# Optimization experiments

Hardware: AMD Instinct MI355X
Metric: run time of the kernel (lower is better)

The kernel has to match this reference:

```python
import jax, jax.numpy as jnp
import numpy as np
from jax import lax

VOCAB = 50257
EMBED = 512
HIDDEN = 1024
SEQ = 512


def setup_inputs() -> dict:
    key = jax.random.key(0)
    ks = jax.random.split(key, 12)
    seq = jax.random.randint(ks[0], (1, SEQ), 0, VOCAB, dtype=jnp.int64 if jax.config.jax_enable_x64 else jnp.int32)
    # h0/c0 emulate xavier_uniform_ init of a [1, hidden] tensor
    bound_hc = float(np.sqrt(6.0 / (1 + HIDDEN)))
    h0 = jax.random.uniform(ks[1], (1, HIDDEN), jnp.float32, -bound_hc, bound_hc)
    c0 = jax.random.uniform(ks[2], (1, HIDDEN), jnp.float32, -bound_hc, bound_hc)
    # parameters
    emb_weight = jax.random.normal(ks[3], (VOCAB, EMBED), jnp.float32)  # nn.Embedding default N(0,1)
    k_lstm = float(1.0 / np.sqrt(HIDDEN))
    w_ih = jax.random.uniform(ks[4], (4 * HIDDEN, 2 * EMBED), jnp.float32, -k_lstm, k_lstm)
    w_hh = jax.random.uniform(ks[5], (4 * HIDDEN, HIDDEN), jnp.float32, -k_lstm, k_lstm)
    b_ih = jax.random.uniform(ks[6], (4 * HIDDEN,), jnp.float32, -k_lstm, k_lstm)
    b_hh = jax.random.uniform(ks[7], (4 * HIDDEN,), jnp.float32, -k_lstm, k_lstm)
    k_lin = k_lstm
    w_lin = jax.random.uniform(ks[8], (VOCAB, HIDDEN), jnp.float32, -k_lin, k_lin)
    b_lin = jax.random.uniform(ks[9], (VOCAB,), jnp.float32, -k_lin, k_lin)
    return {"sequence": seq, "h0": h0, "c0": c0, "emb_weight": emb_weight,
            "w_ih": w_ih, "w_hh": w_hh, "b_ih": b_ih, "b_hh": b_hh,
            "w_lin": w_lin, "b_lin": b_lin}


def _lstm_cell(x, h, c, w_ih, w_hh, b_ih, b_hh):
    # PyTorch LSTMCell gate order: i, f, g, o
    gates = x @ w_ih.T + b_ih + h @ w_hh.T + b_hh  # [1, 4H]
    i, f, g, o = jnp.split(gates, 4, axis=1)
    i = jax.nn.sigmoid(i)
    f = jax.nn.sigmoid(f)
    g = jnp.tanh(g)
    o = jax.nn.sigmoid(o)
    c2 = f * c + i * g
    h2 = o * jnp.tanh(c2)
    return h2, c2


def reference(sequence, h0, c0, emb_weight, w_ih, w_hh, b_ih, b_hh, w_lin, b_lin):
    tokens = sequence[0]  # [S]; module structurally assumes batch=1
    prev0 = jnp.zeros((1, emb_weight.shape[1]), dtype=emb_weight.dtype)
    out0 = jnp.zeros((1, w_lin.shape[0]), dtype=emb_weight.dtype)

    def step(carry, tok):
        h, c, prev, _ = carry
        embed = emb_weight[tok][None, :]                       # [1, E]
        x = jnp.concatenate([prev, embed], axis=1)             # [1, 2E]
        h2, c2 = _lstm_cell(x, h, c, w_ih, w_hh, b_ih, b_hh)
        out = h2 @ w_lin.T + b_lin                             # [1, V]
        prev2 = emb_weight[jnp.argmax(out, axis=1)]            # greedy feedback, [1, E]
        return (h2, c2, prev2, out), None

    (h, c, prev, out), _ = lax.scan(step, (h0, c0, prev0, out0), tokens)
    return out  # logits of the last timestep, [1, VOCAB]
```

## Files before the change

kernel.cpp:

```cpp
#include <hip/hip_runtime.h>
#include <float.h>

#define VOCAB 50257
#define EMBED 512
#define HIDDEN 1024
#define SEQLEN 512
#define XDIM 1024
#define NSW 1571
#define NGW 1024
#define CANDB 128
#define CANDR 512

typedef unsigned long long u64;
typedef unsigned int u32;
typedef unsigned short u16;

__device__ __forceinline__ u32 fmono(float f) {
  u32 b = __float_as_uint(f);
  return b ^ ((b & 0x80000000u) ? 0xFFFFFFFFu : 0x80000000u);
}
__device__ __forceinline__ float funmono(u32 v) {
  u32 b = (v & 0x80000000u) ? (v ^ 0x80000000u) : ~v;
  return __uint_as_float(b);
}

__device__ __forceinline__ float wave_reduce_sum(float v) {
#pragma unroll
  for (int off = 32; off > 0; off >>= 1) v += __shfl_down(v, off);
  return v;
}
__device__ __forceinline__ float wave_reduce_max_f(float v) {
#pragma unroll
  for (int off = 32; off > 0; off >>= 1) v = fmaxf(v, __shfl_down(v, off));
  return v;
}
__device__ __forceinline__ u64 wave_reduce_max_u64(u64 v) {
#pragma unroll
  for (int off = 32; off > 0; off >>= 1) {
    u64 o = __shfl_down(v, off);
    if (o > v) v = o;
  }
  return v;
}

__device__ __forceinline__ float dotf4(float4 a, float4 b) {
  return a.x * b.x + a.y * b.y + a.z * b.z + a.w * b.w;
}

__device__ __forceinline__ int dot4i8(u32 a, u32 b, int c) {
#if __has_builtin(__builtin_amdgcn_sdot4)
  return __builtin_amdgcn_sdot4(a, b, c, false);
#else
  int r = c;
#pragma unroll
  for (int i = 0; i < 4; ++i) {
    const int ai = (int)(a << (24 - 8 * i)) >> 24;
    const int bi = (int)(b << (24 - 8 * i)) >> 24;
    r += ai * bi;
  }
  return r;
#endif
}

__device__ __forceinline__ int q8c(float x, float invs) {
  float q = rintf(x * invs);
  q = fminf(127.0f, fmaxf(-127.0f, q));
  return (int)q;
}


__global__ void init_state(const float* __restrict__ h0, const float* __restrict__ c0,
                           float* __restrict__ hbufs, float* __restrict__ cbufs) {
  int i = threadIdx.x;
  if (i < HIDDEN) {
    hbufs[i] = h0[i];
    cbufs[i] = c0[i];
  }
}

__global__ __launch_bounds__(256)
void convert_i8(const float* __restrict__ wlin, const float* __restrict__ blin,
                u32* __restrict__ qw, float4* __restrict__ rc4) {
  const int row = (blockIdx.x << 2) + (threadIdx.x >> 6);
  const int lane = threadIdx.x & 63;
  if (row >= VOCAB) return;
  const float4* wr = (const float4*)(wlin + (size_t)row * HIDDEN);
  float4 w[4];
#pragma unroll
  for (int i = 0; i < 4; ++i) w[i] = wr[4 * lane + i];
  float m = 0.f;
#pragma unroll
  for (int i = 0; i < 4; ++i)
    m = fmaxf(m, fmaxf(fmaxf(fabsf(w[i].x), fabsf(w[i].y)),
                       fmaxf(fabsf(w[i].z), fabsf(w[i].w))));
  m = wave_reduce_max_f(m);
  m = __shfl(m, 0);
  m = fmaxf(m, 1e-30f);
  const float s_r = m * (1.0f / 127.0f);
  const float invs = 127.0f / m;
  uint4 o;
  float aa = 0.f;
  float dd = 0.f;
  {
    u32 word[4];
#pragma unroll
    for (int i = 0; i < 4; ++i) {
      const int q0 = q8c(w[i].x, invs), q1 = q8c(w[i].y, invs);
      const int q2 = q8c(w[i].z, invs), q3 = q8c(w[i].w, invs);
      aa += (float)(abs(q0) + abs(q1) + abs(q2) + abs(q3));
      const float d0 = w[i].x - s_r * (float)q0, d1 = w[i].y - s_r * (float)q1;
      const float d2 = w[i].z - s_r * (float)q2, d3 = w[i].w - s_r * (float)q3;
      dd += d0 * d0 + d1 * d1 + d2 * d2 + d3 * d3;
      word[i] = (u32)(q0 & 0xFF) | ((u32)(q1 & 0xFF) << 8) |
                ((u32)(q2 & 0xFF) << 16) | ((u32)q3 << 24);
    }
    o.x = word[0]; o.y = word[1]; o.z = word[2]; o.w = word[3];
  }
  ((uint4*)(qw + (size_t)row * 256))[lane] = o;
  aa = wave_reduce_sum(aa);
  dd = wave_reduce_sum(dd);
  if (lane == 0)
    rc4[row] = make_float4(s_r, aa, sqrtf(dd) * 1.0000002f, blin[row]);
}

__global__ __launch_bounds__(256)
void gates_init(const float* __restrict__ wih, const float* __restrict__ whh,
                const float* __restrict__ bih, const float* __restrict__ bhh,
                const float* __restrict__ emb, const int* __restrict__ seq,
                const float* __restrict__ hbufs, float* __restrict__ gp) {
  __shared__ __align__(16) float xs2[EMBED];
  __shared__ __align__(16) float hs2[HIDDEN];
  const int tid = threadIdx.x;
  const int lane = tid & 63;
  const int wid = tid >> 6;
  const int tok = seq[0];
  for (int i = tid; i < EMBED; i += 256) xs2[i] = emb[(size_t)tok * EMBED + i];
  for (int i = tid; i < HIDDEN; i += 256) hs2[i] = hbufs[i];
  __syncthreads();

  const int row = (blockIdx.x << 2) + wid;
  const float4* wr = (const float4*)(wih + (size_t)row * XDIM);
  const float4* hr = (const float4*)(whh + (size_t)row * HIDDEN);
  float a = 0.f;
#pragma unroll
  for (int i = 0; i < 2; ++i) {
    const int k = lane + i * 64;
    a += dotf4(wr[128 + k], *((const float4*)&xs2[k * 4]));
  }
#pragma unroll
  for (int i = 0; i < 4; ++i) {
    const int k = lane + i * 64;
    a += dotf4(hr[k], *((const float4*)&hs2[k * 4]));
  }
  a = wave_reduce_sum(a);
  if (lane == 0) gp[row] = a + bih[row] + bhh[row];
}


__global__ __launch_bounds__(256)
void lstm_thin(const float* __restrict__ emb, const float* __restrict__ wih,
               const float* __restrict__ wlin, const float* __restrict__ blin,
               const float* __restrict__ gp,
               float* __restrict__ hbufs, float* __restrict__ cbufs,
               const u64* __restrict__ slotLo, const float* __restrict__ slotUp,
               const float* __restrict__ Lb, int t) {
  __shared__ __align__(16) float xs[EMBED];
  __shared__ __align__(16) float hs[HIDDEN];
  __shared__ u64 mred[4];
  __shared__ u64 bred[4];
  __shared__ int listb[CANDB];
  __shared__ int listr[CANDR];
  __shared__ int cntb, cntr;
  __shared__ int ptokS;

  const int tid = threadIdx.x;
  const int lane = tid & 63;
  const int wid = tid >> 6;

  const float* hin = hbufs + (t & 1) * HIDDEN;
  const float* cin = cbufs + (t & 1) * HIDDEN;
  float* hout = hbufs + ((t + 1) & 1) * HIDDEN;
  float* cout = cbufs + ((t + 1) & 1) * HIDDEN;

  const u64* sLo = slotLo + ((t + 1) & 1) * NSW;
  const float* sUp = slotUp + ((t + 1) & 1) * NSW;

  const int j = (blockIdx.x << 2) + wid;

  float4 wv[8];
  if (t > 0) {
#pragma unroll
    for (int g = 0; g < 4; ++g) {
      const float4* wr = (const float4*)(wih + (size_t)(g * HIDDEN + j) * XDIM);
      wv[2 * g] = wr[lane];
      wv[2 * g + 1] = wr[lane + 64];
    }
  }

  u64 v = 0;
  if (t > 0) {
#pragma unroll
    for (int k = 0; k < 7; ++k) {
      const int i = tid + (k << 8);
      if (i < NSW) {
        const u64 p = sLo[i];
        if (p > v) v = p;
      }
    }
  }

  ((float4*)hs)[tid] = ((const float4*)hin)[tid];

  int ptok = 0;
  if (t > 0) {
    v = wave_reduce_max_u64(v);
    if (lane == 0) mred[wid] = v;
    if (tid == 0) { cntb = 0; cntr = 0; }
    __syncthreads();
    u64 m = mred[0];
    if (mred[1] > m) m = mred[1];
    if (mred[2] > m) m = mred[2];
    if (mred[3] > m) m = mred[3];
    const float thrv = funmono((u32)(m >> 32));

#pragma unroll
    for (int k = 0; k < 7; ++k) {
      const int i = tid + (k << 8);
      if (i < NSW && sUp[i] >= thrv) {
        int ix = atomicAdd(&cntb, 1);
        if (ix < CANDB) listb[ix] = i;
      }
    }
    __syncthreads();
    const int nb = (cntb < CANDB) ? cntb : CANDB;

    for (int idx = tid; idx < nb * 32; idx += 256) {
      const int row = listb[idx >> 5] * 32 + (idx & 31);
      if (row < VOCAB && Lb[row] >= thrv) {
        int ix = atomicAdd(&cntr, 1);
        if (ix < CANDR) listr[ix] = row;
      }
    }
    __syncthreads();
    const int nr = (cntr < CANDR) ? cntr : CANDR;

    u64 best = 0;
    for (int ci = wid; ci < nr; ci += 4) {
      const int row = listr[ci];
      const float4* wr = (const float4*)(wlin + (size_t)row * HIDDEN);
      float a = 0.f;
#pragma unroll
      for (int i = 0; i < 4; ++i) {
        const int k = lane + i * 64;
        a += dotf4(wr[k], *((const float4*)&hs[k * 4]));
      }
      a = wave_reduce_sum(a);
      if (lane == 0) {
        const u64 pk = ((u64)fmono(a + blin[row]) << 32) | (u32)(VOCAB - row);
        if (pk > best) best = pk;
      }
    }
    if (lane == 0) bred[wid] = best;
    __syncthreads();
    if (tid == 0) {
      u64 b = bred[0];
      if (bred[1] > b) b = bred[1];
      if (bred[2] > b) b = bred[2];
      if (bred[3] > b) b = bred[3];
      ptokS = VOCAB - (int)(u32)(b & 0xFFFFFFFFu);
    }
    __syncthreads();
    ptok = ptokS;
  }

  if (t > 0) {
    for (int i = tid; i < EMBED; i += 256) xs[i] = emb[(size_t)ptok * EMBED + i];
  }
  __syncthreads();

  float ag[4] = {0.f, 0.f, 0.f, 0.f};
  if (t > 0) {
    const float4 xv0 = *((const float4*)&xs[lane * 4]);
    const float4 xv1 = *((const float4*)&xs[(lane + 64) * 4]);
#pragma unroll
    for (int g = 0; g < 4; ++g)
      ag[g] = dotf4(wv[2 * g], xv0) + dotf4(wv[2 * g + 1], xv1);
#pragma unroll
    for (int off = 32; off > 0; off >>= 1) {
#pragma unroll
      for (int g = 0; g < 4; ++g) ag[g] += __shfl_down(ag[g], off);
    }
  }

  if (lane == 0) {
    const float gi = gp[j] + ag[0];
    const float gf = gp[HIDDEN + j] + ag[1];
    const float gg = gp[2 * HIDDEN + j] + ag[2];
    const float go = gp[3 * HIDDEN + j] + ag[3];
    const float si = 1.0f / (1.0f + expf(-gi));
    const float sf = 1.0f / (1.0f + expf(-gf));
    const float tg = tanhf(gg);
    const float so = 1.0f / (1.0f + expf(-go));
    const float c2 = sf * cin[j] + si * tg;
    const float h2 = so * tanhf(c2);
    cout[j] = c2;
    hout[j] = h2;
  }
}

__global__ __launch_bounds__(256, 4)
void screen_gp(const u32* __restrict__ qw, const float4* __restrict__ rc4,
               const float* __restrict__ wih, const float* __restrict__ whh,
               const float* __restrict__ bih, const float* __restrict__ bhh,
               const float* __restrict__ emb, const int* __restrict__ seq,
               const float* __restrict__ hbufs, float* __restrict__ Lb,
               u64* __restrict__ slotLo, float* __restrict__ slotUp,
               float* __restrict__ gp, int t) {
  __shared__ __align__(16) float4 hs4[256];
  __shared__ __align__(16) u32 qhw[256];
  __shared__ __align__(16) u32 qh2w[256];
  __shared__ __align__(16) float xs2[EMBED];
  __shared__ float redm[4], reda[4], reds[4];
  __shared__ u64 redLo[4];
  __shared__ float redUp[4];

  const int tid = threadIdx.x;
  const int lane = tid & 63;
  const int wid = tid >> 6;
  const int bid = blockIdx.x;
  const int par = t & 1;

  const float* h = hbufs + ((t + 1) & 1) * HIDDEN;

  if (bid < NSW) {
    const float4 hv = ((const float4*)h)[tid];
    float m = fmaxf(fmaxf(fabsf(hv.x), fabsf(hv.y)), fmaxf(fabsf(hv.z), fabsf(hv.w)));
    float sa = fabsf(hv.x) + fabsf(hv.y) + fabsf(hv.z) + fabsf(hv.w);
    float ss = dotf4(hv, hv);
    m = wave_reduce_max_f(m);
    sa = wave_reduce_sum(sa);
    ss = wave_reduce_sum(ss);
    if (lane == 0) { redm[wid] = m; reda[wid] = sa; reds[wid] = ss; }
    __syncthreads();
    float maxh = fmaxf(fmaxf(redm[0], redm[1]), fmaxf(redm[2], redm[3]));
    maxh = fmaxf(maxh, 1e-30f);
    const float SumAbsH = reda[0] + reda[1] + reda[2] + reda[3];
    const float NormH = sqrtf(reds[0] + reds[1] + reds[2] + reds[3]) * 1.0000002f;
    const float s_h = maxh * (1.0f / 127.0f);
    const float s2 = s_h * (1.0f / 254.0f);
    const float inv_sh = 127.0f / maxh;
    const float inv_s2 = 254.0f * inv_sh;
    {
      const int qa = q8c(hv.x, inv_sh), qb = q8c(hv.y, inv_sh);
      const int qc = q8c(hv.z, inv_sh), qd = q8c(hv.w, inv_sh);
      const float ra = hv.x - s_h * (float)qa, rb = hv.y - s_h * (float)qb;
      const float rcr = hv.z - s_h * (float)qc, rd = hv.w - s_h * (float)qd;
      const int pa = q8c(ra, inv_s2), pb = q8c(rb, inv_s2);
      const int pc = q8c(rcr, inv_s2), pd = q8c(rd, inv_s2);
      qhw[tid] = (u32)(qa & 0xFF) | ((u32)(qb & 0xFF) << 8) |
                 ((u32)(qc & 0xFF) << 16) | ((u32)qd << 24);
      qh2w[tid] = (u32)(pa & 0xFF) | ((u32)(pb & 0xFF) << 8) |
                  ((u32)(pc & 0xFF) << 16) | ((u32)pd << 24);
    }
    __syncthreads();
    const uint4 qh = ((const uint4*)qhw)[lane];
    const uint4 qh2 = ((const uint4*)qh2w)[lane];

    const int row0 = bid * 32 + wid * 8;
    uint4 wq[8];
    const uint4 z4 = make_uint4(0u, 0u, 0u, 0u);
#pragma unroll
    for (int r = 0; r < 8; ++r) {
      const int row = row0 + r;
      wq[r] = (row < VOCAB) ? ((const uint4*)(qw + (size_t)row * 256))[lane] : z4;
    }
    float4 rcv[8];
    if (lane == 0) {
#pragma unroll
      for (int r = 0; r < 8; ++r) {
        const int row = row0 + r;
        rcv[r] = (row < VOCAB) ? rc4[row] : make_float4(0.f, 0.f, 0.f, 0.f);
      }
    }
    int a1[8], a2[8];
#pragma unroll
    for (int r = 0; r < 8; ++r) {
      a1[r] = dot4i8(wq[r].w, qh.w,
              dot4i8(wq[r].z, qh.z, dot4i8(wq[r].y, qh.y, dot4i8(wq[r].x, qh.x, 0))));
      a2[r] = dot4i8(wq[r].w, qh2.w,
              dot4i8(wq[r].z, qh2.z, dot4i8(wq[r].y, qh2.y, dot4i8(wq[r].x, qh2.x, 0))));
    }
#pragma unroll
    for (int off = 32; off > 0; off >>= 1) {
#pragma unroll
      for (int r = 0; r < 8; ++r) {
        a1[r] += __shfl_down(a1[r], off);
        a2[r] += __shfl_down(a2[r], off);
      }
    }
    if (lane == 0) {
      u64 lmax = 0;
      float umax = -FLT_MAX;
#pragma unroll
      for (int r = 0; r < 8; ++r) {
        const int row = row0 + r;
        if (row < VOCAB) {
          const float s_r = rcv[r].x;
          const float Lq = s_r * (s_h * (float)a1[r] + s2 * (float)a2[r]) + rcv[r].w;
          const float wside = fminf(0.5f * s_r * SumAbsH, rcv[r].z * NormH);
          const float er = wside + s_r * rcv[r].y * (0.5f * s2) + 1e-3f;
          const float up = Lq + er;
          const float lo = Lq - er;
          Lb[row] = up;
          const u64 pk = ((u64)fmono(lo) << 32) | (u32)(VOCAB - row);
          if (pk > lmax) lmax = pk;
          if (up > umax) umax = up;
        }
      }
      redLo[wid] = lmax;
      redUp[wid] = umax;
    }
    __syncthreads();
    if (tid == 0) {
      u64 a = redLo[0];
      if (redLo[1] > a) a = redLo[1];
      if (redLo[2] > a) a = redLo[2];
      if (redLo[3] > a) a = redLo[3];
      float b = fmaxf(fmaxf(redUp[0], redUp[1]), fmaxf(redUp[2], redUp[3]));
      slotLo[par * NSW + bid] = a;
      slotUp[par * NSW + bid] = b;
    }
  } else {
    const int tok = seq[t + 1];
    hs4[tid] = ((const float4*)h)[tid];
    for (int i = tid; i < EMBED; i += 256) xs2[i] = emb[(size_t)tok * EMBED + i];
    __syncthreads();

    const int row = ((bid - NSW) << 2) + wid;
    const float4* wr = (const float4*)(wih + (size_t)row * XDIM);
    const float4* hr = (const float4*)(whh + (size_t)row * HIDDEN);
    float a = 0.f;
#pragma unroll
    for (int i = 0; i < 2; ++i) {
      const int k = lane + i * 64;
      a += dotf4(wr[128 + k], *((const float4*)&xs2[k * 4]));
    }
#pragma unroll
    for (int i = 0; i < 4; ++i) {
      const int k = lane + i * 64;
      a += dotf4(hr[k], hs4[k]);
    }
    a = wave_reduce_sum(a);
    if (lane == 0) gp[row] = a + bih[row] + bhh[row];
  }
}

__global__ __launch_bounds__(256)
void logits_out(const float* __restrict__ wlin, const float* __restrict__ blin,
                const float* __restrict__ h, float* __restrict__ out) {
  __shared__ __align__(16) float hs[HIDDEN];
  const int tid = threadIdx.x;
  const int lane = tid & 63;
  const int wid = tid >> 6;
  for (int i = tid; i < HIDDEN; i += 256) hs[i] = h[i];
  __syncthreads();
  const int row = blockIdx.x * 4 + wid;
  if (row < VOCAB) {
    const float4* wr = (const float4*)(wlin + (size_t)row * HIDDEN);
    float a = 0.f;
#pragma unroll
    for (int i = 0; i < 4; ++i) {
      const int k = lane + i * 64;
      a += dotf4(wr[k], *((const float4*)&hs[k * 4]));
    }
    a = wave_reduce_sum(a);
    if (lane == 0) out[row] = a + blin[row];
  }
}


__global__ void init_state_v0(const float* __restrict__ h0, const float* __restrict__ c0,
                              float* __restrict__ hbufs, float* __restrict__ cbufs,
                              u64* __restrict__ partials) {
  int i = threadIdx.x;
  if (i < HIDDEN) {
    hbufs[i] = h0[i];
    cbufs[i] = c0[i];
  }
  if (i < 512) partials[i] = 0ull;
}

__global__ __launch_bounds__(256)
void lstm_step_v0(const float* __restrict__ emb,
                  const float* __restrict__ wih, const float* __restrict__ whh,
                  const float* __restrict__ bih, const float* __restrict__ bhh,
                  const int* __restrict__ seq,
                  float* __restrict__ hbufs, float* __restrict__ cbufs,
                  u64* __restrict__ partials, int t) {
  __shared__ __align__(16) float xs[XDIM];
  __shared__ __align__(16) float hs[HIDDEN];
  __shared__ u64 red[4];
  __shared__ int ptok_s;

  const int tid = threadIdx.x;
  const int lane = tid & 63;
  const int wid = tid >> 6;

  const float* hin = hbufs + (t & 1) * HIDDEN;
  const float* cin = cbufs + (t & 1) * HIDDEN;
  float* hout = hbufs + ((t + 1) & 1) * HIDDEN;
  float* cout = cbufs + ((t + 1) & 1) * HIDDEN;

  int ptok = -1;
  if (t > 0) {
    const u64* part = partials + ((t + 1) & 1) * 256;
    u64 v = wave_reduce_max_u64(part[tid]);
    if (lane == 0) red[wid] = v;
    __syncthreads();
    if (tid == 0) {
      u64 m = red[0];
      if (red[1] > m) m = red[1];
      if (red[2] > m) m = red[2];
      if (red[3] > m) m = red[3];
      ptok_s = VOCAB - (int)(u32)(m & 0xFFFFFFFFu);
    }
    __syncthreads();
    ptok = ptok_s;
  }
  if (blockIdx.x == 0) partials[(t & 1) * 256 + tid] = 0ull;

  const int tok = seq[t];
  for (int i = tid; i < EMBED; i += 256) {
    xs[i] = (t == 0) ? 0.0f : emb[(size_t)ptok * EMBED + i];
    xs[EMBED + i] = emb[(size_t)tok * EMBED + i];
  }
  for (int i = tid; i < HIDDEN; i += 256) hs[i] = hin[i];
  __syncthreads();

  const int j = blockIdx.x * 4 + wid;
  float acc[4];
#pragma unroll
  for (int g = 0; g < 4; ++g) {
    const float4* wx = (const float4*)(wih + (size_t)(g * HIDDEN + j) * XDIM);
    const float4* wh = (const float4*)(whh + (size_t)(g * HIDDEN + j) * HIDDEN);
    float a = 0.f;
#pragma unroll
    for (int i = 0; i < 4; ++i) {
      const int k = lane + i * 64;
      a += dotf4(wx[k], *((const float4*)&xs[k * 4]));
      a += dotf4(wh[k], *((const float4*)&hs[k * 4]));
    }
    acc[g] = wave_reduce_sum(a);
  }

  if (lane == 0) {
    float gi = acc[0] + bih[j] + bhh[j];
    float gf = acc[1] + bih[HIDDEN + j] + bhh[HIDDEN + j];
    float gg = acc[2] + bih[2 * HIDDEN + j] + bhh[2 * HIDDEN + j];
    float go = acc[3] + bih[3 * HIDDEN + j] + bhh[3 * HIDDEN + j];
    float si = 1.0f / (1.0f + expf(-gi));
    float sf = 1.0f / (1.0f + expf(-gf));
    float tg = tanhf(gg);
    float so = 1.0f / (1.0f + expf(-go));
    float c2 = sf * cin[j] + si * tg;
    float h2 = so * tanhf(c2);
    cout[j] = c2;
    hout[j] = h2;
  }
}

__global__ __launch_bounds__(256)
void logits_step_v0(const float* __restrict__ wlin, const float* __restrict__ blin,
                    const float* __restrict__ hbufs, float* __restrict__ out,
                    u64* __restrict__ partials, int t) {
  __shared__ __align__(16) float hs[HIDDEN];
  __shared__ u64 red[4];
  const int tid = threadIdx.x;
  const int lane = tid & 63;
  const int wid = tid >> 6;

  const float* h = hbufs + ((t + 1) & 1) * HIDDEN;
  for (int i = tid; i < HIDDEN; i += 256) hs[i] = h[i];
  __syncthreads();

  const int row = blockIdx.x * 4 + wid;
  u64 pk = 0ull;
  if (row < VOCAB) {
    const float4* wr = (const float4*)(wlin + (size_t)row * HIDDEN);
    float a = 0.f;
#pragma unroll
    for (int i = 0; i < 4; ++i) {
      const int k = lane + i * 64;
      a += dotf4(wr[k], *((const float4*)&hs[k * 4]));
    }
    a = wave_reduce_sum(a);
    if (lane == 0) {
      float logit = a + blin[row];
      out[row] = logit;
      pk = ((u64)fmono(logit) << 32) | (u32)(VOCAB - row);
    }
  }
  if (lane == 0) red[wid] = pk;
  __syncthreads();
  if (tid == 0) {
    u64 m = red[0];
    if (red[1] > m) m = red[1];
    if (red[2] > m) m = red[2];
    if (red[3] > m) m = red[3];
    atomicMax(&partials[(t & 1) * 256 + (blockIdx.x & 255)], m);
  }
}

extern "C" void kernel_launch(void* const* d_in, const int* in_sizes, int n_in,
                              void* d_out, int out_size, void* d_ws, size_t ws_size,
                              hipStream_t stream) {
  const int* seq = (const int*)d_in[0];
  const float* h0 = (const float*)d_in[1];
  const float* c0 = (const float*)d_in[2];
  const float* emb = (const float*)d_in[3];
  const float* wih = (const float*)d_in[4];
  const float* whh = (const float*)d_in[5];
  const float* bih = (const float*)d_in[6];
  const float* bhh = (const float*)d_in[7];
  const float* wlin = (const float*)d_in[8];
  const float* blin = (const float*)d_in[9];
  float* out = (float*)d_out;

  const size_t OFF_SL = 0;
  const size_t OFF_SU = 25600;
  const size_t OFF_H = OFF_SU + 12800;
  const size_t OFF_C = OFF_H + 8192;
  const size_t OFF_GP = OFF_C + 8192;
  const size_t OFF_LB = OFF_GP + 16384;
  const size_t OFF_RC = OFF_LB + 201216;
  const size_t OFF_QW = OFF_RC + 804352;
  const size_t NEED = OFF_QW + (size_t)VOCAB * 1024;

  u64* slotLo = (u64*)((char*)d_ws + OFF_SL);
  float* slotUp = (float*)((char*)d_ws + OFF_SU);
  float* hbufs = (float*)((char*)d_ws + OFF_H);
  float* cbufs = (float*)((char*)d_ws + OFF_C);
  float* gp = (float*)((char*)d_ws + OFF_GP);
  float* Lb = (float*)((char*)d_ws + OFF_LB);
  float4* rc4 = (float4*)((char*)d_ws + OFF_RC);
  u32* qw = (u32*)((char*)d_ws + OFF_QW);

  if (ws_size >= NEED) {
    init_state<<<1, 1024, 0, stream>>>(h0, c0, hbufs, cbufs);
    convert_i8<<<(VOCAB + 3) / 4, 256, 0, stream>>>(wlin, blin, qw, rc4);
    gates_init<<<NGW, 256, 0, stream>>>(wih, whh, bih, bhh, emb, seq, hbufs, gp);
    for (int t = 0; t < SEQLEN; ++t) {
      lstm_thin<<<HIDDEN / 4, 256, 0, stream>>>(emb, wih, wlin, blin, gp,
                                                hbufs, cbufs, slotLo, slotUp,
                                                Lb, t);
      if (t < SEQLEN - 1)
        screen_gp<<<NSW + NGW, 256, 0, stream>>>(qw, rc4, wih, whh, bih, bhh,
                                                 emb, seq, hbufs, Lb, slotLo,
                                                 slotUp, gp, t);
    }
    logits_out<<<(VOCAB + 3) / 4, 256, 0, stream>>>(wlin, blin, hbufs, out);
  } else {
    u64* p0 = (u64*)d_ws;
    float* hb0 = (float*)((char*)d_ws + 4096);
    float* cb0 = hb0 + 2 * HIDDEN;
    init_state_v0<<<1, 1024, 0, stream>>>(h0, c0, hb0, cb0, p0);
    for (int t = 0; t < SEQLEN; ++t) {
      lstm_step_v0<<<HIDDEN / 4, 256, 0, stream>>>(emb, wih, whh, bih, bhh, seq,
                                                   hb0, cb0, p0, t);
      logits_step_v0<<<(VOCAB + 3) / 4, 256, 0, stream>>>(wlin, blin, hb0, out,
                                                          p0, t);
    }
  }
}
```

Baseline: 17.76 ms.

## Precompute token-embedding gate contributions for all steps; spread LSTM cell over more blocks

Adds a gates_tok kernel that computes the known-token half of the input projection plus both biases for every timestep up front into an 8MB workspace buffer. screen_gp then only does the recurrent h·W_hh product and adds the precomputed term, dropping the per-step embedding load and W_ih half-dot. lstm_thin now runs one block per hidden unit with one gate per wave, so the feedback-embedding dot is spread over 4x more blocks. The cost is an extra prologue pass, more workspace, and a block-level sync plus a redundant argmax-candidate scan in each of 4x more blocks per step.

```diff
diff --git a/kernel.cpp b/kernel.cpp
--- a/kernel.cpp
+++ b/kernel.cpp
@@ -121,6 +121,27 @@
   dd = wave_reduce_sum(dd);
   if (lane == 0)
     rc4[row] = make_float4(s_r, aa, sqrtf(dd) * 1.0000002f, blin[row]);
+}
+
+__global__ __launch_bounds__(256)
+void gates_tok(const float* __restrict__ wih,
+               const float* __restrict__ bih, const float* __restrict__ bhh,
+               const float* __restrict__ emb, const int* __restrict__ seq,
+               float* __restrict__ gpc) {
+  const int lane = threadIdx.x & 63;
+  const int wid = threadIdx.x >> 6;
+  const int row = wid * HIDDEN + blockIdx.x;
+  const float4* wr = (const float4*)(wih + (size_t)row * XDIM);
+  const float4 w0 = wr[128 + lane];
+  const float4 w1 = wr[128 + lane + 64];
+  const float bb = bih[row] + bhh[row];
+  for (int t = 0; t < SEQLEN; ++t) {
+    const int tok = seq[t];
+    const float4* er = (const float4*)(emb + (size_t)tok * EMBED);
+    float a = dotf4(w0, er[lane]) + dotf4(w1, er[lane + 64]);
+    a = wave_reduce_sum(a);
+    if (lane == 0) gpc[t * 4096 + row] = a + bb;
+  }
 }
 
 __global__ __launch_bounds__(256)
@@ -168,6 +189,7 @@
   __shared__ __align__(16) float hs[HIDDEN];
   __shared__ u64 mred[4];
   __shared__ u64 bred[4];
+  __shared__ float gl[4];
   __shared__ int listb[CANDB];
   __shared__ int listr[CANDR];
   __shared__ int cntb, cntr;
@@ -176,6 +198,7 @@
   const int tid = threadIdx.x;
   const int lane = tid & 63;
   const int wid = tid >> 6;
+  const int j = blockIdx.x;
 
   const float* hin = hbufs + (t & 1) * HIDDEN;
   const float* cin = cbufs + (t & 1) * HIDDEN;
@@ -185,16 +208,11 @@
   const u64* sLo = slotLo + ((t + 1) & 1) * NSW;
   const float* sUp = slotUp + ((t + 1) & 1) * NSW;
 
-  const int j = (blockIdx.x << 2) + wid;
-
-  float4 wv[8];
+  float4 wv0, wv1;
   if (t > 0) {
-#pragma unroll
-    for (int g = 0; g < 4; ++g) {
-      const float4* wr = (const float4*)(wih + (size_t)(g * HIDDEN + j) * XDIM);
-      wv[2 * g] = wr[lane];
-      wv[2 * g + 1] = wr[lane + 64];
-    }
+    const float4* wr = (const float4*)(wih + (size_t)(wid * HIDDEN + j) * XDIM);
+    wv0 = wr[lane];
+    wv1 = wr[lane + 64];
   }
 
   u64 v = 0;
@@ -278,25 +296,21 @@
   }
   __syncthreads();
 
-  float ag[4] = {0.f, 0.f, 0.f, 0.f};
+  float ag = 0.f;
   if (t > 0) {
     const float4 xv0 = *((const float4*)&xs[lane * 4]);
     const float4 xv1 = *((const float4*)&xs[(lane + 64) * 4]);
-#pragma unroll
-    for (int g = 0; g < 4; ++g)
-      ag[g] = dotf4(wv[2 * g], xv0) + dotf4(wv[2 * g + 1], xv1);
-#pragma unroll
-    for (int off = 32; off > 0; off >>= 1) {
-#pragma unroll
-      for (int g = 0; g < 4; ++g) ag[g] += __shfl_down(ag[g], off);
-    }
-  }
-
-  if (lane == 0) {
-    const float gi = gp[j] + ag[0];
-    const float gf = gp[HIDDEN + j] + ag[1];
-    const float gg = gp[2 * HIDDEN + j] + ag[2];
-    const float go = gp[3 * HIDDEN + j] + ag[3];
+    ag = dotf4(wv0, xv0) + dotf4(wv1, xv1);
+    ag = wave_reduce_sum(ag);
+  }
+  if (lane == 0) gl[wid] = ag;
+  __syncthreads();
+
+  if (tid == 0) {
+    const float gi = gp[j] + gl[0];
+    const float gf = gp[HIDDEN + j] + gl[1];
+    const float gg = gp[2 * HIDDEN + j] + gl[2];
+    const float go = gp[3 * HIDDEN + j] + gl[3];
     const float si = 1.0f / (1.0f + expf(-gi));
     const float sf = 1.0f / (1.0f + expf(-gf));
     const float tg = tanhf(gg);
@@ -310,16 +324,13 @@
 
 __global__ __launch_bounds__(256, 4)
 void screen_gp(const u32* __restrict__ qw, const float4* __restrict__ rc4,
-               const float* __restrict__ wih, const float* __restrict__ whh,
-               const float* __restrict__ bih, const float* __restrict__ bhh,
-               const float* __restrict__ emb, const int* __restrict__ seq,
+               const float* __restrict__ whh, const float* __restrict__ gpc,
                const float* __restrict__ hbufs, float* __restrict__ Lb,
                u64* __restrict__ slotLo, float* __restrict__ slotUp,
                float* __restrict__ gp, int t) {
   __shared__ __align__(16) float4 hs4[256];
   __shared__ __align__(16) u32 qhw[256];
   __shared__ __align__(16) u32 qh2w[256];
-  __shared__ __align__(16) float xs2[EMBED];
   __shared__ float redm[4], reda[4], reds[4];
   __shared__ u64 redLo[4];
   __shared__ float redUp[4];
@@ -431,27 +442,19 @@
       slotUp[par * NSW + bid] = b;
     }
   } else {
-    const int tok = seq[t + 1];
     hs4[tid] = ((const float4*)h)[tid];
-    for (int i = tid; i < EMBED; i += 256) xs2[i] = emb[(size_t)tok * EMBED + i];
     __syncthreads();
 
     const int row = ((bid - NSW) << 2) + wid;
-    const float4* wr = (const float4*)(wih + (size_t)row * XDIM);
     const float4* hr = (const float4*)(whh + (size_t)row * HIDDEN);
     float a = 0.f;
-#pragma unroll
-    for (int i = 0; i < 2; ++i) {
-      const int k = lane + i * 64;
-      a += dotf4(wr[128 + k], *((const float4*)&xs2[k * 4]));
-    }
 #pragma unroll
     for (int i = 0; i < 4; ++i) {
       const int k = lane + i * 64;
       a += dotf4(hr[k], hs4[k]);
     }
     a = wave_reduce_sum(a);
-    if (lane == 0) gp[row] = a + bih[row] + bhh[row];
+    if (lane == 0) gp[row] = a + gpc[(t + 1) * 4096 + row];
   }
 }
 
@@ -633,7 +636,8 @@
   const size_t OFF_GP = OFF_C + 8192;
   const size_t OFF_LB = OFF_GP + 16384;
   const size_t OFF_RC = OFF_LB + 201216;
-  const size_t OFF_QW = OFF_RC + 804352;
+  const size_t OFF_GPC = OFF_RC + 804352;
+  const size_t OFF_QW = OFF_GPC + 8388608;
   const size_t NEED = OFF_QW + (size_t)VOCAB * 1024;
 
   u64* slotLo = (u64*)((char*)d_ws + OFF_SL);
@@ -643,20 +647,21 @@
   float* gp = (float*)((char*)d_ws + OFF_GP);
   float* Lb = (float*)((char*)d_ws + OFF_LB);
   float4* rc4 = (float4*)((char*)d_ws + OFF_RC);
+  float* gpc = (float*)((char*)d_ws + OFF_GPC);
   u32* qw = (u32*)((char*)d_ws + OFF_QW);
 
   if (ws_size >= NEED) {
     init_state<<<1, 1024, 0, stream>>>(h0, c0, hbufs, cbufs);
     convert_i8<<<(VOCAB + 3) / 4, 256, 0, stream>>>(wlin, blin, qw, rc4);
+    gates_tok<<<1024, 256, 0, stream>>>(wih, bih, bhh, emb, seq, gpc);
     gates_init<<<NGW, 256, 0, stream>>>(wih, whh, bih, bhh, emb, seq, hbufs, gp);
     for (int t = 0; t < SEQLEN; ++t) {
-      lstm_thin<<<HIDDEN / 4, 256, 0, stream>>>(emb, wih, wlin, blin, gp,
-                                                hbufs, cbufs, slotLo, slotUp,
-                                                Lb, t);
+      lstm_thin<<<HIDDEN, 256, 0, stream>>>(emb, wih, wlin, blin, gp,
+                                            hbufs, cbufs, slotLo, slotUp,
+                                            Lb, t);
       if (t < SEQLEN - 1)
-        screen_gp<<<NSW + NGW, 256, 0, stream>>>(qw, rc4, wih, whh, bih, bhh,
-                                                 emb, seq, hbufs, Lb, slotLo,
-                                                 slotUp, gp, t);
+        screen_gp<<<NSW + NGW, 256, 0, stream>>>(qw, rc4, whh, gpc, hbufs,
+                                                 Lb, slotLo, slotUp, gp, t);
     }
     logits_out<<<(VOCAB + 3) / 4, 256, 0, stream>>>(wlin, blin, hbufs, out);
   } else {
```

After: 18.13 ms. 1.02x slower.

## Precompute token-embedding gate contributions for all steps before the recurrent loop

Applied to the files above, without the earlier changes.

Adds a gates_tok kernel that computes the W_ih·embed(token)+biases part of the gates for every timestep up front, since it does not depend on the recurrence, and stores it in a new workspace buffer. The per-step screen_gp gate blocks then only do the W_hh·h product, two rows per wave with half as many blocks, which removes the per-step embedding load and half the weight traffic. The int8 screening dot products are now converted to float and scaled before the shuffle reduction, halving the number of shuffles, and the screening error margin is widened slightly to cover the extra float rounding. The cost is roughly 8 MB more workspace and one extra upfront kernel.

```diff
diff --git a/kernel.cpp b/kernel.cpp
--- a/kernel.cpp
+++ b/kernel.cpp
@@ -8,6 +8,7 @@
 #define XDIM 1024
 #define NSW 1571
 #define NGW 1024
+#define NGW2 512
 #define CANDB 128
 #define CANDR 512
 
@@ -121,6 +122,27 @@
   dd = wave_reduce_sum(dd);
   if (lane == 0)
     rc4[row] = make_float4(s_r, aa, sqrtf(dd) * 1.0000002f, blin[row]);
+}
+
+__global__ __launch_bounds__(256)
+void gates_tok(const float* __restrict__ wih,
+               const float* __restrict__ bih, const float* __restrict__ bhh,
+               const float* __restrict__ emb, const int* __restrict__ seq,
+               float* __restrict__ gpc) {
+  const int lane = threadIdx.x & 63;
+  const int wid = threadIdx.x >> 6;
+  const int row = wid * HIDDEN + blockIdx.x;
+  const float4* wr = (const float4*)(wih + (size_t)row * XDIM);
+  const float4 w0 = wr[128 + lane];
+  const float4 w1 = wr[128 + lane + 64];
+  const float bb = bih[row] + bhh[row];
+  for (int t = 0; t < SEQLEN; ++t) {
+    const int tok = seq[t];
+    const float4* er = (const float4*)(emb + (size_t)tok * EMBED);
+    float a = dotf4(w0, er[lane]) + dotf4(w1, er[lane + 64]);
+    a = wave_reduce_sum(a);
+    if (lane == 0) gpc[t * 4096 + row] = a + bb;
+  }
 }
 
 __global__ __launch_bounds__(256)
@@ -176,6 +198,7 @@
   const int tid = threadIdx.x;
   const int lane = tid & 63;
   const int wid = tid >> 6;
+  const int j = (blockIdx.x << 2) + wid;
 
   const float* hin = hbufs + (t & 1) * HIDDEN;
   const float* cin = cbufs + (t & 1) * HIDDEN;
@@ -184,8 +207,6 @@
 
   const u64* sLo = slotLo + ((t + 1) & 1) * NSW;
   const float* sUp = slotUp + ((t + 1) & 1) * NSW;
-
-  const int j = (blockIdx.x << 2) + wid;
 
   float4 wv[8];
   if (t > 0) {
@@ -310,16 +331,13 @@
 
 __global__ __launch_bounds__(256, 4)
 void screen_gp(const u32* __restrict__ qw, const float4* __restrict__ rc4,
-               const float* __restrict__ wih, const float* __restrict__ whh,
-               const float* __restrict__ bih, const float* __restrict__ bhh,
-               const float* __restrict__ emb, const int* __restrict__ seq,
+               const float* __restrict__ whh, const float* __restrict__ gpc,
                const float* __restrict__ hbufs, float* __restrict__ Lb,
                u64* __restrict__ slotLo, float* __restrict__ slotUp,
                float* __restrict__ gp, int t) {
   __shared__ __align__(16) float4 hs4[256];
   __shared__ __align__(16) u32 qhw[256];
   __shared__ __align__(16) u32 qh2w[256];
-  __shared__ __align__(16) float xs2[EMBED];
   __shared__ float redm[4], reda[4], reds[4];
   __shared__ u64 redLo[4];
   __shared__ float redUp[4];
@@ -382,21 +400,19 @@
         rcv[r] = (row < VOCAB) ? rc4[row] : make_float4(0.f, 0.f, 0.f, 0.f);
       }
     }
-    int a1[8], a2[8];
+    float fo[8];
 #pragma unroll
     for (int r = 0; r < 8; ++r) {
-      a1[r] = dot4i8(wq[r].w, qh.w,
-              dot4i8(wq[r].z, qh.z, dot4i8(wq[r].y, qh.y, dot4i8(wq[r].x, qh.x, 0))));
-      a2[r] = dot4i8(wq[r].w, qh2.w,
-              dot4i8(wq[r].z, qh2.z, dot4i8(wq[r].y, qh2.y, dot4i8(wq[r].x, qh2.x, 0))));
+      const int a1 = dot4i8(wq[r].w, qh.w,
+                     dot4i8(wq[r].z, qh.z, dot4i8(wq[r].y, qh.y, dot4i8(wq[r].x, qh.x, 0))));
+      const int a2 = dot4i8(wq[r].w, qh2.w,
+                     dot4i8(wq[r].z, qh2.z, dot4i8(wq[r].y, qh2.y, dot4i8(wq[r].x, qh2.x, 0))));
+      fo[r] = s_h * (float)a1 + s2 * (float)a2;
     }
 #pragma unroll
     for (int off = 32; off > 0; off >>= 1) {
 #pragma unroll
-      for (int r = 0; r < 8; ++r) {
-        a1[r] += __shfl_down(a1[r], off);
-        a2[r] += __shfl_down(a2[r], off);
-      }
+      for (int r = 0; r < 8; ++r) fo[r] += __shfl_down(fo[r], off);
     }
     if (lane == 0) {
       u64 lmax = 0;
@@ -406,9 +422,9 @@
         const int row = row0 + r;
         if (row < VOCAB) {
           const float s_r = rcv[r].x;
-          const float Lq = s_r * (s_h * (float)a1[r] + s2 * (float)a2[r]) + rcv[r].w;
+          const float Lq = s_r * fo[r] + rcv[r].w;
           const float wside = fminf(0.5f * s_r * SumAbsH, rcv[r].z * NormH);
-          const float er = wside + s_r * rcv[r].y * (0.5f * s2) + 1e-3f;
+          const float er = wside + s_r * rcv[r].y * (0.5f * s2) + 1.5e-3f;
           const float up = Lq + er;
           const float lo = Lq - er;
           Lb[row] = up;
@@ -431,27 +447,23 @@
       slotUp[par * NSW + bid] = b;
     }
   } else {
-    const int tok = seq[t + 1];
     hs4[tid] = ((const float4*)h)[tid];
-    for (int i = tid; i < EMBED; i += 256) xs2[i] = emb[(size_t)tok * EMBED + i];
-    __syncthreads();
-
-    const int row = ((bid - NSW) << 2) + wid;
-    const float4* wr = (const float4*)(wih + (size_t)row * XDIM);
-    const float4* hr = (const float4*)(whh + (size_t)row * HIDDEN);
-    float a = 0.f;
-#pragma unroll
-    for (int i = 0; i < 2; ++i) {
-      const int k = lane + i * 64;
-      a += dotf4(wr[128 + k], *((const float4*)&xs2[k * 4]));
-    }
-#pragma unroll
-    for (int i = 0; i < 4; ++i) {
-      const int k = lane + i * 64;
-      a += dotf4(hr[k], hs4[k]);
-    }
-    a = wave_reduce_sum(a);
-    if (lane == 0) gp[row] = a + bih[row] + bhh[row];
+    __syncthreads();
+
+    const int row0 = ((bid - NSW) << 3) + (wid << 1);
+#pragma unroll
+    for (int rr = 0; rr < 2; ++rr) {
+      const int row = row0 + rr;
+      const float4* hr = (const float4*)(whh + (size_t)row * HIDDEN);
+      float a = 0.f;
+#pragma unroll
+      for (int i = 0; i < 4; ++i) {
+        const int k = lane + i * 64;
+        a += dotf4(hr[k], hs4[k]);
+      }
+      a = wave_reduce_sum(a);
+      if (lane == 0) gp[row] = a + gpc[(t + 1) * 4096 + row];
+    }
   }
 }
 
@@ -633,7 +645,8 @@
   const size_t OFF_GP = OFF_C + 8192;
   const size_t OFF_LB = OFF_GP + 16384;
   const size_t OFF_RC = OFF_LB + 201216;
-  const size_t OFF_QW = OFF_RC + 804352;
+  const size_t OFF_GPC = OFF_RC + 804352;
+  const size_t OFF_QW = OFF_GPC + 8388608;
   const size_t NEED = OFF_QW + (size_t)VOCAB * 1024;
 
   u64* slotLo = (u64*)((char*)d_ws + OFF_SL);
@@ -643,20 +656,21 @@
   float* gp = (float*)((char*)d_ws + OFF_GP);
   float* Lb = (float*)((char*)d_ws + OFF_LB);
   float4* rc4 = (float4*)((char*)d_ws + OFF_RC);
+  float* gpc = (float*)((char*)d_ws + OFF_GPC);
   u32* qw = (u32*)((char*)d_ws + OFF_QW);
 
   if (ws_size >= NEED) {
     init_state<<<1, 1024, 0, stream>>>(h0, c0, hbufs, cbufs);
     convert_i8<<<(VOCAB + 3) / 4, 256, 0, stream>>>(wlin, blin, qw, rc4);
+    gates_tok<<<1024, 256, 0, stream>>>(wih, bih, bhh, emb, seq, gpc);
     gates_init<<<NGW, 256, 0, stream>>>(wih, whh, bih, bhh, emb, seq, hbufs, gp);
     for (int t = 0; t < SEQLEN; ++t) {
       lstm_thin<<<HIDDEN / 4, 256, 0, stream>>>(emb, wih, wlin, blin, gp,
                                                 hbufs, cbufs, slotLo, slotUp,
                                                 Lb, t);
       if (t < SEQLEN - 1)
-        screen_gp<<<NSW + NGW, 256, 0, stream>>>(qw, rc4, wih, whh, bih, bhh,
-                                                 emb, seq, hbufs, Lb, slotLo,
-                                                 slotUp, gp, t);
+        screen_gp<<<NSW + NGW2, 256, 0, stream>>>(qw, rc4, whh, gpc, hbufs,
+                                                  Lb, slotLo, slotUp, gp, t);
     }
     logits_out<<<(VOCAB + 3) / 4, 256, 0, stream>>>(wlin, blin, hbufs, out);
   } else {
```

Result: faster. 16.96 ms (-4.5%).
